# Performance work log

Hardware: AMD Instinct MI355X
Metric: run time of the kernel (lower is better)

The kernel has to match this reference:

```python
import jax, jax.numpy as jnp
import numpy as np

H_SIZE = 1024
N_HEADS = 16
D_K = H_SIZE // N_HEADS


def setup_inputs() -> dict:
    key = jax.random.key(0)
    ks = jax.random.split(key, 12)
    s = 1.0 / np.sqrt(H_SIZE)
    inp = {
        "x": jax.random.normal(ks[0], (2, 2048, H_SIZE), dtype=jnp.float32),
        "Wq": jax.random.uniform(ks[1], (H_SIZE, H_SIZE), minval=-s, maxval=s),
        "bq": jax.random.uniform(ks[2], (H_SIZE,), minval=-s, maxval=s),
        "Wk": jax.random.uniform(ks[3], (H_SIZE, H_SIZE), minval=-s, maxval=s),
        "bk": jax.random.uniform(ks[4], (H_SIZE,), minval=-s, maxval=s),
        "Wv": jax.random.uniform(ks[5], (H_SIZE, H_SIZE), minval=-s, maxval=s),
        "bv": jax.random.uniform(ks[6], (H_SIZE,), minval=-s, maxval=s),
        "Wo": jax.random.uniform(ks[7], (H_SIZE, H_SIZE), minval=-s, maxval=s),
        "bo": jax.random.uniform(ks[8], (H_SIZE,), minval=-s, maxval=s),
        "ln_gamma": jnp.ones((H_SIZE,), dtype=jnp.float32),
        "ln_beta": jnp.zeros((H_SIZE,), dtype=jnp.float32),
    }
    return inp


def reference(x, Wq, bq, Wk, bk, Wv, bv, Wo, bo, ln_gamma, ln_beta):
    B, L, H = x.shape
    residual = x
    # QKV projections -> [B, n_heads, L, d_k]
    def proj(W, b):
        return (x @ W.T + b).reshape(B, L, N_HEADS, D_K).transpose(0, 2, 1, 3)
    q = proj(Wq, bq)
    k = proj(Wk, bk)
    v = proj(Wv, bv)
    # scaled dot-product attention (dropout = identity in eval mode)
    scores = jnp.einsum("bhqd,bhkd->bhqk", q, k) / jnp.sqrt(jnp.float32(D_K))
    attn = jax.nn.softmax(scores, axis=-1)
    out = jnp.einsum("bhqk,bhkd->bhqd", attn, v)
    out = out.transpose(0, 2, 1, 3).reshape(B, L, H)
    out = out @ Wo.T + bo
    # residual + LayerNorm
    y = out + residual
    mu = jnp.mean(y, axis=-1, keepdims=True)
    var = jnp.var(y, axis=-1, keepdims=True)
    y = (y - mu) / jnp.sqrt(var + 1e-5) * ln_gamma + ln_beta
    return y
```

## Files before the change

### kernel.cpp

```cpp
#include <hip/hip_runtime.h>

#define H_SIZE 1024
#define N_HEADS 16
#define D_K 64
#define SEQ 2048
#define BATCH 2
#define M_TOT 4096

typedef __bf16 __attribute__((ext_vector_type(8))) bf16_8;
typedef float __attribute__((ext_vector_type(4))) f32x4;
typedef float __attribute__((ext_vector_type(16))) f32x16;
typedef int __attribute__((ext_vector_type(4))) int4v;

#define SWZ(r) ((((r) & 7) ^ (((r) >> 3) & 7)))

__device__ __forceinline__ ushort f2bf(float f) {
    unsigned int u = __float_as_uint(f);
    unsigned int r = (u + 0x7FFFu + ((u >> 16) & 1u)) >> 16;
    return (ushort)r;
}

__device__ __forceinline__ unsigned int cvtpk(float lo, float hi) {
    unsigned int r;
    asm("v_cvt_pk_bf16_f32 %0, %1, %2" : "=v"(r) : "v"(lo), "v"(hi));
    return r;
}

__device__ __forceinline__ float exp2_raw(float x) {
    float r;
    asm("v_exp_f32 %0, %1" : "=v"(r) : "v"(x));
    return r;
}

__device__ __forceinline__ void gld16(void* lds, const void* g) {
    __builtin_amdgcn_global_load_lds(
        (const __attribute__((address_space(1))) unsigned int*)g,
        (__attribute__((address_space(3))) unsigned int*)lds, 16, 0, 0);
}

__global__ __launch_bounds__(256) void cast_all_kernel(
    const float* __restrict__ x, const float* __restrict__ wq, const float* __restrict__ wk,
    const float* __restrict__ wv, const float* __restrict__ wo,
    ushort* __restrict__ xb, ushort* __restrict__ wqb, ushort* __restrict__ wkb,
    ushort* __restrict__ wvb, ushort* __restrict__ wob) {
    int i = blockIdx.x * 256 + threadIdx.x;
    const float* src;
    ushort* dst;
    int off;
    if (i < 1048576) {
        src = x; dst = xb; off = i;
    } else {
        int j = i - 1048576;
        int w = j >> 18;
        off = j & 262143;
        src = (w == 0) ? wq : (w == 1) ? wk : (w == 2) ? wv : wo;
        dst = (w == 0) ? wqb : (w == 1) ? wkb : (w == 2) ? wvb : wob;
    }
    float4 v = ((const float4*)src)[off];
    ushort4 o;
    o.x = f2bf(v.x); o.y = f2bf(v.y); o.z = f2bf(v.z); o.w = f2bf(v.w);
    ((ushort4*)dst)[off] = o;
}

__global__ __launch_bounds__(256) void gemm_qkv(
    const ushort* __restrict__ A, const ushort* __restrict__ wq,
    const ushort* __restrict__ wk, const ushort* __restrict__ wv,
    const float* __restrict__ bq, const float* __restrict__ bk, const float* __restrict__ bv,
    ushort* __restrict__ Qb, ushort* __restrict__ Kb, ushort* __restrict__ Vtb) {
    constexpr int BK = 32;
    __shared__ ushort As[3][128 * BK];
    __shared__ ushort Bs[3][128 * BK];
    const int tid = threadIdx.x;
    const int lane = tid & 63, wid = tid >> 6;
    const int wr = wid >> 1, wc = wid & 1;
    const int hi = lane >> 4, lo = lane & 15;
    const int bm0 = blockIdx.x * 128;
    const int t3 = blockIdx.y >> 3;
    const int bn0 = (blockIdx.y & 7) * 128;
    const ushort* Bw = (t3 == 0) ? wq : (t3 == 1) ? wk : wv;
    const float* bias = (t3 == 0) ? bq : (t3 == 1) ? bk : bv;

    f32x4 acc[4][4] = {};

    const int srow = tid >> 2;
    const int sseg = ((tid & 3) ^ ((tid >> 3) & 3)) * 8;
    const ushort* gaB = A + (size_t)(bm0 + srow) * H_SIZE + sseg;
    const ushort* gbB = Bw + (size_t)(bn0 + srow) * H_SIZE + sseg;
    const int ldsOff = tid * 16;

#define STAGE(ba, bb, kt)                                 \
    {                                                     \
        char* la = (char*)(ba) + ldsOff;                  \
        char* lb = (char*)(bb) + ldsOff;                  \
        gld16(la, gaB + (kt));                            \
        gld16(la + 4096, gaB + 64 * H_SIZE + (kt));       \
        gld16(lb, gbB + (kt));                            \
        gld16(lb + 4096, gbB + 64 * H_SIZE + (kt));       \
    }

    STAGE(&As[0][0], &Bs[0][0], 0);
    STAGE(&As[1][0], &Bs[1][0], BK);
    asm volatile("s_waitcnt vmcnt(4)" ::: "memory");
    __builtin_amdgcn_s_barrier();
    __builtin_amdgcn_sched_barrier(0);

    constexpr int NT = H_SIZE / BK;
    const int rxv = (lo >> 1) & 3;
    int cur = 0;
    for (int t = 0; t < NT; t++) {
        int c2 = cur + 2; if (c2 >= 3) c2 -= 3;
        if (t + 2 < NT) STAGE(&As[c2][0], &Bs[c2][0], (t + 2) * BK);
        {
            bf16_8 af[4], bfv[4];
            const ushort* pa = &As[cur][(wr * 64 + lo) * BK + ((hi ^ rxv) * 8)];
            const ushort* pb = &Bs[cur][(wc * 64 + lo) * BK + ((hi ^ rxv) * 8)];
#pragma unroll
            for (int i = 0; i < 4; i++) af[i] = *(const bf16_8*)(pa + i * 16 * BK);
#pragma unroll
            for (int i = 0; i < 4; i++) bfv[i] = *(const bf16_8*)(pb + i * 16 * BK);
#pragma unroll
            for (int mi = 0; mi < 4; mi++)
#pragma unroll
                for (int ni = 0; ni < 4; ni++)
                    acc[mi][ni] = __builtin_amdgcn_mfma_f32_16x16x32_bf16(
                        af[mi], bfv[ni], acc[mi][ni], 0, 0, 0);
        }
        if (t + 1 < NT) {
            if (t + 2 < NT) { asm volatile("s_waitcnt vmcnt(4)" ::: "memory"); }
            else            { asm volatile("s_waitcnt vmcnt(0)" ::: "memory"); }
            __builtin_amdgcn_s_barrier();
            __builtin_amdgcn_sched_barrier(0);
        }
        cur = cur + 1; if (cur >= 3) cur -= 3;
    }
#undef STAGE

#pragma unroll
    for (int mi = 0; mi < 4; mi++) {
#pragma unroll
        for (int ni = 0; ni < 4; ni++) {
            const int row0 = bm0 + wr * 64 + mi * 16 + hi * 4;
            const int col = bn0 + wc * 64 + ni * 16 + lo;
            const float bv = bias[col];
            const int h = col >> 6, dk = col & 63;
            if (t3 == 2) {
                const int b = row0 >> 11, l0 = row0 & 2047;
                const int lsw0 = (l0 & ~63) | (((((l0 >> 3) & 7) ^ SWZ(dk)) & 7) << 3) | (l0 & 7);
                uint2 o;
                o.x = cvtpk(acc[mi][ni][0] + bv, acc[mi][ni][1] + bv);
                o.y = cvtpk(acc[mi][ni][2] + bv, acc[mi][ni][3] + bv);
                *(uint2*)&Vtb[((size_t)(b * N_HEADS + h) * D_K + dk) * SEQ + lsw0] = o;
            } else {
#pragma unroll
                for (int rr = 0; rr < 4; rr++) {
                    const int m = row0 + rr;
                    const int b = m >> 11, l = m & 2047;
                    float val = acc[mi][ni][rr] + bv;
                    if (t3 == 0) {
                        Qb[((size_t)(b * N_HEADS + h) * SEQ + l) * D_K + dk] =
                            f2bf(val * 0.18033688f);
                    } else {
                        int dks = ((((dk >> 3) ^ SWZ(l & 63)) & 7) << 3) | (dk & 7);
                        Kb[((size_t)(b * N_HEADS + h) * SEQ + l) * D_K + dks] = f2bf(val);
                    }
                }
            }
        }
    }
}

__global__ __launch_bounds__(256) void gemm_o(const ushort* __restrict__ A,
                                              const ushort* __restrict__ Bw,
                                              const float* __restrict__ bias,
                                              const float* __restrict__ resid,
                                              float* __restrict__ outp) {
    constexpr int BK = 32;
    __shared__ ushort As[3][128 * BK];
    __shared__ ushort Bs[3][64 * BK];
    const int tid = threadIdx.x;
    const int lane = tid & 63, wid = tid >> 6;
    const int wr = wid >> 1, wc = wid & 1;
    const int hi = lane >> 4, lo = lane & 15;
    const int bm0 = blockIdx.x * 128, bn0 = blockIdx.y * 64;

    f32x4 acc[4][2] = {};

    const int srow = tid >> 2;
    const int sseg = ((tid & 3) ^ ((tid >> 3) & 3)) * 8;
    const ushort* gaB = A + (size_t)(bm0 + srow) * H_SIZE + sseg;
    const ushort* gbB = Bw + (size_t)(bn0 + srow) * H_SIZE + sseg;
    const int ldsOff = tid * 16;

#define STAGE(ba, bb, kt)                                 \
    {                                                     \
        char* la = (char*)(ba) + ldsOff;                  \
        gld16(la, gaB + (kt));                            \
        gld16(la + 4096, gaB + 64 * H_SIZE + (kt));       \
        gld16((char*)(bb) + ldsOff, gbB + (kt));          \
    }

    STAGE(&As[0][0], &Bs[0][0], 0);
    STAGE(&As[1][0], &Bs[1][0], BK);
    asm volatile("s_waitcnt vmcnt(3)" ::: "memory");
    __builtin_amdgcn_s_barrier();
    __builtin_amdgcn_sched_barrier(0);

    constexpr int NT = H_SIZE / BK;
    const int rxv = (lo >> 1) & 3;
    int cur = 0;
    for (int t = 0; t < NT; t++) {
        int c2 = cur + 2; if (c2 >= 3) c2 -= 3;
        if (t + 2 < NT) STAGE(&As[c2][0], &Bs[c2][0], (t + 2) * BK);
        {
            bf16_8 af[4], bfv[2];
            const ushort* pa = &As[cur][(wr * 64 + lo) * BK + ((hi ^ rxv) * 8)];
            const ushort* pb = &Bs[cur][(wc * 32 + lo) * BK + ((hi ^ rxv) * 8)];
#pragma unroll
            for (int i = 0; i < 4; i++) af[i] = *(const bf16_8*)(pa + i * 16 * BK);
#pragma unroll
            for (int i = 0; i < 2; i++) bfv[i] = *(const bf16_8*)(pb + i * 16 * BK);
#pragma unroll
            for (int mi = 0; mi < 4; mi++)
#pragma unroll
                for (int ni = 0; ni < 2; ni++)
                    acc[mi][ni] = __builtin_amdgcn_mfma_f32_16x16x32_bf16(
                        af[mi], bfv[ni], acc[mi][ni], 0, 0, 0);
        }
        if (t + 1 < NT) {
            if (t + 2 < NT) { asm volatile("s_waitcnt vmcnt(3)" ::: "memory"); }
            else            { asm volatile("s_waitcnt vmcnt(0)" ::: "memory"); }
            __builtin_amdgcn_s_barrier();
            __builtin_amdgcn_sched_barrier(0);
        }
        cur = cur + 1; if (cur >= 3) cur -= 3;
    }
#undef STAGE

#pragma unroll
    for (int mi = 0; mi < 4; mi++) {
#pragma unroll
        for (int ni = 0; ni < 2; ni++) {
            const int row0 = bm0 + wr * 64 + mi * 16 + hi * 4;
            const int col = bn0 + wc * 32 + ni * 16 + lo;
            const float bv = bias[col];
#pragma unroll
            for (int rr = 0; rr < 4; rr++) {
                const int m = row0 + rr;
                outp[(size_t)m * H_SIZE + col] =
                    acc[mi][ni][rr] + bv + resid[(size_t)m * H_SIZE + col];
            }
        }
    }
}

__global__ __launch_bounds__(256) void attn_kernel(const ushort* __restrict__ Q,
                                                   const ushort* __restrict__ Ksw,
                                                   const ushort* __restrict__ Vsw,
                                                   ushort* __restrict__ Op0,
                                                   ushort* __restrict__ Op1,
                                                   float* __restrict__ Lpart) {
    __shared__ ushort Ks[2][64 * 64];
    __shared__ ushort Vs[2][64 * 64];
    const int lane = threadIdx.x & 63, wid = threadIdx.x >> 6;
    const int h32 = lane >> 5, q32 = lane & 31;
    const int bh = blockIdx.y;
    const int z = blockIdx.z;
    const int q0w = blockIdx.x * 128 + wid * 32;
    const int kbase = z * (SEQ / 2);
    const ushort* Qh = Q + (size_t)bh * SEQ * D_K;
    const ushort* Kp = Ksw + (size_t)bh * SEQ * D_K;
    const ushort* Vp = Vsw + (size_t)bh * D_K * SEQ;

    bf16_8 qf[4];
#pragma unroll
    for (int tt = 0; tt < 4; tt++)
        qf[tt] = *(const bf16_8*)(Qh + (size_t)(q0w + q32) * D_K + tt * 16 + h32 * 8);

    bf16_8 onesf;
#pragma unroll
    for (int i = 0; i < 8; i++) onesf[i] = (__bf16)1.0f;

    f32x16 oacc0 = {}, oacc1 = {}, lsacc = {};

    const int koff = wid * 2048 + lane * 16;
    const int vrow = wid * 16 + (lane >> 3);
    const int vseg = (lane & 7) * 16;

#define STAGE(bb, kt)                                                             \
    {                                                                             \
        const char* kg = (const char*)(Kp + (size_t)(kt) * D_K);                  \
        char* kl = (char*)&Ks[bb][0];                                             \
        gld16(kl + koff, kg + koff);                                              \
        gld16(kl + koff + 1024, kg + koff + 1024);                                \
        char* vl = (char*)&Vs[bb][0];                                             \
        gld16(vl + vrow * 128 + vseg,                                             \
              (const char*)(Vp + (size_t)vrow * SEQ + (kt)) + vseg);              \
        gld16(vl + (vrow + 8) * 128 + vseg,                                       \
              (const char*)(Vp + (size_t)(vrow + 8) * SEQ + (kt)) + vseg);        \
    }

    STAGE(0, kbase);
    __syncthreads();
    int buf = 0;
    constexpr int NTT = (SEQ / 2) / 64;
    for (int t = 0; t < NTT; t++) {
        if (t + 1 < NTT) STAGE(buf ^ 1, kbase + (t + 1) * 64);
        const ushort* kb = &Ks[buf][0];
        const ushort* vb = &Vs[buf][0];
#pragma unroll
        for (int kh = 0; kh < 2; kh++) {
            f32x16 st = {};
            const int krow = kh * 32 + q32;
            __builtin_amdgcn_s_setprio(1);
#pragma unroll
            for (int tt = 0; tt < 4; tt++) {
                int sg = (2 * tt + h32) ^ SWZ(krow);
                bf16_8 kf = *(const bf16_8*)(kb + krow * 64 + sg * 8);
                st = __builtin_amdgcn_mfma_f32_32x32x16_bf16(kf, qf[tt], st, 0, 0, 0);
            }
            __builtin_amdgcn_s_setprio(0);
            float p[16];
#pragma unroll
            for (int rr = 0; rr < 16; rr++) p[rr] = exp2_raw(st[rr]);

            union { unsigned int w[4]; bf16_8 v; } pf0, pf1;
#pragma unroll
            for (int i = 0; i < 2; i++) {
                unsigned int a = cvtpk(p[2 * i], p[2 * i + 1]);
                unsigned int b = cvtpk(p[4 + 2 * i], p[4 + 2 * i + 1]);
                asm volatile("v_permlane32_swap_b32 %0, %1" : "+v"(a), "+v"(b));
                pf0.w[i] = a; pf0.w[2 + i] = b;
                unsigned int c = cvtpk(p[8 + 2 * i], p[8 + 2 * i + 1]);
                unsigned int d = cvtpk(p[12 + 2 * i], p[12 + 2 * i + 1]);
                asm volatile("v_permlane32_swap_b32 %0, %1" : "+v"(c), "+v"(d));
                pf1.w[i] = c; pf1.w[2 + i] = d;
            }

            __builtin_amdgcn_s_setprio(1);
            lsacc = __builtin_amdgcn_mfma_f32_32x32x16_bf16(pf0.v, onesf, lsacc, 0, 0, 0);
            lsacc = __builtin_amdgcn_mfma_f32_32x32x16_bf16(pf1.v, onesf, lsacc, 0, 0, 0);
            {
                const int vr0 = q32;
                int sg0 = (4 * kh + h32) ^ SWZ(vr0);
                int sg1 = (4 * kh + 2 + h32) ^ SWZ(vr0);
                bf16_8 vf0 = *(const bf16_8*)(vb + vr0 * 64 + sg0 * 8);
                bf16_8 vf1 = *(const bf16_8*)(vb + vr0 * 64 + sg1 * 8);
                oacc0 = __builtin_amdgcn_mfma_f32_32x32x16_bf16(pf0.v, vf0, oacc0, 0, 0, 0);
                oacc0 = __builtin_amdgcn_mfma_f32_32x32x16_bf16(pf1.v, vf1, oacc0, 0, 0, 0);
            }
            {
                const int vr1 = 32 + q32;
                int sg0 = (4 * kh + h32) ^ SWZ(vr1);
                int sg1 = (4 * kh + 2 + h32) ^ SWZ(vr1);
                bf16_8 vf0 = *(const bf16_8*)(vb + vr1 * 64 + sg0 * 8);
                bf16_8 vf1 = *(const bf16_8*)(vb + vr1 * 64 + sg1 * 8);
                oacc1 = __builtin_amdgcn_mfma_f32_32x32x16_bf16(pf0.v, vf0, oacc1, 0, 0, 0);
                oacc1 = __builtin_amdgcn_mfma_f32_32x32x16_bf16(pf1.v, vf1, oacc1, 0, 0, 0);
            }
            __builtin_amdgcn_s_setprio(0);
        }
        __syncthreads();
        buf ^= 1;
    }
#undef STAGE

    ushort* Op = (z == 0) ? Op0 : Op1;
    float* Lp = Lpart + (size_t)z * N_HEADS * BATCH * SEQ;
    const int b = bh >> 4, h = bh & 15;
#pragma unroll
    for (int rr = 0; rr < 16; rr++) {
        const int qloc = (rr & 3) + 8 * (rr >> 2) + 4 * h32;
        const int l = q0w + qloc;
        ushort* orow = Op + ((size_t)(b * SEQ + l)) * H_SIZE + h * 64;
        orow[q32] = f2bf(oacc0[rr]);
        orow[32 + q32] = f2bf(oacc1[rr]);
        if (q32 == 0) Lp[(size_t)bh * SEQ + l] = lsacc[rr];
    }
}

__global__ __launch_bounds__(256) void combine_kernel(const ushort* __restrict__ O0,
                                                      const ushort* __restrict__ O1,
                                                      const float* __restrict__ Lp,
                                                      ushort* __restrict__ Ao) {
    int idx = blockIdx.x * 256 + threadIdx.x;
    int m = idx >> 7;
    int col0 = (idx & 127) * 8;
    int b = m >> 11, l = m & 2047, h = col0 >> 6;
    int bh = b * N_HEADS + h;
    float inv = 1.0f / (Lp[(size_t)bh * SEQ + l] +
                        Lp[(size_t)(N_HEADS * BATCH + bh) * SEQ + l]);
    size_t off = (size_t)m * H_SIZE + col0;
    int4v a = *(const int4v*)(O0 + off);
    int4v c = *(const int4v*)(O1 + off);
    unsigned int r[4];
#pragma unroll
    for (int j = 0; j < 4; j++) {
        unsigned int ua = (unsigned int)a[j], uc = (unsigned int)c[j];
        float lo = __uint_as_float(ua << 16) + __uint_as_float(uc << 16);
        float hi = __uint_as_float(ua & 0xFFFF0000u) + __uint_as_float(uc & 0xFFFF0000u);
        r[j] = cvtpk(lo * inv, hi * inv);
    }
    *(int4v*)(Ao + off) = *(const int4v*)r;
}

__global__ __launch_bounds__(256) void ln_kernel(float* __restrict__ y,
                                                 const float* __restrict__ gamma,
                                                 const float* __restrict__ beta) {
    const int row = blockIdx.x;
    float4* p = (float4*)(y + (size_t)row * H_SIZE);
    float4 v = p[threadIdx.x];
    float s = v.x + v.y + v.z + v.w;
    float s2 = v.x * v.x + v.y * v.y + v.z * v.z + v.w * v.w;
#pragma unroll
    for (int off = 1; off < 64; off <<= 1) {
        s += __shfl_xor(s, off);
        s2 += __shfl_xor(s2, off);
    }
    __shared__ float ss[4], ss2[4];
    const int wid = threadIdx.x >> 6, lane = threadIdx.x & 63;
    if (lane == 0) { ss[wid] = s; ss2[wid] = s2; }
    __syncthreads();
    s = ss[0] + ss[1] + ss[2] + ss[3];
    s2 = ss2[0] + ss2[1] + ss2[2] + ss2[3];
    const float mean = s * (1.0f / H_SIZE);
    const float var = s2 * (1.0f / H_SIZE) - mean * mean;
    const float rstd = rsqrtf(var + 1e-5f);
    const float4 g = ((const float4*)gamma)[threadIdx.x];
    const float4 bt = ((const float4*)beta)[threadIdx.x];
    float4 o;
    o.x = (v.x - mean) * rstd * g.x + bt.x;
    o.y = (v.y - mean) * rstd * g.y + bt.y;
    o.z = (v.z - mean) * rstd * g.z + bt.z;
    o.w = (v.w - mean) * rstd * g.w + bt.w;
    p[threadIdx.x] = o;
}

extern "C" void kernel_launch(void* const* d_in, const int* in_sizes, int n_in,
                              void* d_out, int out_size, void* d_ws, size_t ws_size,
                              hipStream_t stream) {
    const float* x = (const float*)d_in[0];
    const float* Wq = (const float*)d_in[1];
    const float* bq = (const float*)d_in[2];
    const float* Wk = (const float*)d_in[3];
    const float* bk = (const float*)d_in[4];
    const float* Wv = (const float*)d_in[5];
    const float* bv = (const float*)d_in[6];
    const float* Wo = (const float*)d_in[7];
    const float* bo = (const float*)d_in[8];
    const float* gamma = (const float*)d_in[9];
    const float* beta = (const float*)d_in[10];

    char* ws = (char*)d_ws;
    ushort* xb  = (ushort*)(ws);
    ushort* wqb = (ushort*)(ws + (8u << 20));
    ushort* wkb = (ushort*)(ws + (10u << 20));
    ushort* wvb = (ushort*)(ws + (12u << 20));
    ushort* wob = (ushort*)(ws + (14u << 20));
    ushort* Qb  = (ushort*)(ws + (16u << 20));
    ushort* Kb  = (ushort*)(ws + (24u << 20));
    ushort* Vtb = (ushort*)(ws + (32u << 20));
    ushort* Ao  = (ushort*)(ws + (40u << 20));
    ushort* Op0 = (ushort*)(ws);
    ushort* Op1 = Ao;
    float*  Lpt = (float*)(ws + (48u << 20));

    cast_all_kernel<<<8192, 256, 0, stream>>>(x, Wq, Wk, Wv, Wo, xb, wqb, wkb, wvb, wob);

    dim3 gq(M_TOT / 128, 24);
    gemm_qkv<<<gq, 256, 0, stream>>>(xb, wqb, wkb, wvb, bq, bk, bv, Qb, Kb, Vtb);

    dim3 g2(SEQ / 128, BATCH * N_HEADS, 2);
    attn_kernel<<<g2, 256, 0, stream>>>(Qb, Kb, Vtb, Op0, Op1, Lpt);

    combine_kernel<<<(M_TOT * H_SIZE / 8) / 256, 256, 0, stream>>>(Op0, Op1, Lpt, Ao);

    dim3 go(M_TOT / 128, H_SIZE / 64);
    gemm_o<<<go, 256, 0, stream>>>(Ao, wob, bo, x, (float*)d_out);

    ln_kernel<<<M_TOT, 256, 0, stream>>>((float*)d_out, gamma, beta);
}
```

Measured before the change: 142.4 us.

## Process two query tiles per wave with triple-buffered K/V and VALU row sums

Each wave now handles 64 query rows instead of 32, reusing every K and V fragment loaded from LDS across two query tiles and halving the grid. The K/V staging moves from double to triple buffering with explicit vmcnt waits and raw barriers, so loads run two tiles ahead. The softmax denominator is now summed on the VALU with a cross-half shuffle instead of extra MFMAs against a ones vector. In exchange the kernel needs more registers and LDS per block, and with only 512 blocks occupancy and load balance across CUs may drop.

```diff
diff --git a/kernel.cpp b/kernel.cpp
--- a/kernel.cpp
+++ b/kernel.cpp
@@ -259,28 +259,27 @@
                                                    ushort* __restrict__ Op0,
                                                    ushort* __restrict__ Op1,
                                                    float* __restrict__ Lpart) {
-    __shared__ ushort Ks[2][64 * 64];
-    __shared__ ushort Vs[2][64 * 64];
+    __shared__ ushort Ks[3][64 * 64];
+    __shared__ ushort Vs[3][64 * 64];
     const int lane = threadIdx.x & 63, wid = threadIdx.x >> 6;
     const int h32 = lane >> 5, q32 = lane & 31;
     const int bh = blockIdx.y;
     const int z = blockIdx.z;
-    const int q0w = blockIdx.x * 128 + wid * 32;
+    const int q0w = blockIdx.x * 256 + wid * 64;
     const int kbase = z * (SEQ / 2);
     const ushort* Qh = Q + (size_t)bh * SEQ * D_K;
     const ushort* Kp = Ksw + (size_t)bh * SEQ * D_K;
     const ushort* Vp = Vsw + (size_t)bh * D_K * SEQ;
 
-    bf16_8 qf[4];
-#pragma unroll
-    for (int tt = 0; tt < 4; tt++)
-        qf[tt] = *(const bf16_8*)(Qh + (size_t)(q0w + q32) * D_K + tt * 16 + h32 * 8);
-
-    bf16_8 onesf;
-#pragma unroll
-    for (int i = 0; i < 8; i++) onesf[i] = (__bf16)1.0f;
-
-    f32x16 oacc0 = {}, oacc1 = {}, lsacc = {};
+    bf16_8 qfA[4], qfB[4];
+#pragma unroll
+    for (int tt = 0; tt < 4; tt++) {
+        qfA[tt] = *(const bf16_8*)(Qh + (size_t)(q0w + q32) * D_K + tt * 16 + h32 * 8);
+        qfB[tt] = *(const bf16_8*)(Qh + (size_t)(q0w + 32 + q32) * D_K + tt * 16 + h32 * 8);
+    }
+
+    f32x16 oA0 = {}, oA1 = {}, oB0 = {}, oB1 = {};
+    float lsA = 0.f, lsB = 0.f;
 
     const int koff = wid * 2048 + lane * 16;
     const int vrow = wid * 16 + (lane >> 3);
@@ -300,53 +299,75 @@
     }
 
     STAGE(0, kbase);
-    __syncthreads();
-    int buf = 0;
+    STAGE(1, kbase + 64);
+    asm volatile("s_waitcnt vmcnt(4)" ::: "memory");
+    __builtin_amdgcn_s_barrier();
+    __builtin_amdgcn_sched_barrier(0);
+
     constexpr int NTT = (SEQ / 2) / 64;
+    int cur = 0;
     for (int t = 0; t < NTT; t++) {
-        if (t + 1 < NTT) STAGE(buf ^ 1, kbase + (t + 1) * 64);
-        const ushort* kb = &Ks[buf][0];
-        const ushort* vb = &Vs[buf][0];
+        int c2 = cur + 2; if (c2 >= 3) c2 -= 3;
+        if (t + 2 < NTT) STAGE(c2, kbase + (t + 2) * 64);
+        const ushort* kb = &Ks[cur][0];
+        const ushort* vb = &Vs[cur][0];
 #pragma unroll
         for (int kh = 0; kh < 2; kh++) {
-            f32x16 st = {};
+            f32x16 stA = {}, stB = {};
             const int krow = kh * 32 + q32;
             __builtin_amdgcn_s_setprio(1);
 #pragma unroll
             for (int tt = 0; tt < 4; tt++) {
                 int sg = (2 * tt + h32) ^ SWZ(krow);
                 bf16_8 kf = *(const bf16_8*)(kb + krow * 64 + sg * 8);
-                st = __builtin_amdgcn_mfma_f32_32x32x16_bf16(kf, qf[tt], st, 0, 0, 0);
+                stA = __builtin_amdgcn_mfma_f32_32x32x16_bf16(kf, qfA[tt], stA, 0, 0, 0);
+                stB = __builtin_amdgcn_mfma_f32_32x32x16_bf16(kf, qfB[tt], stB, 0, 0, 0);
             }
             __builtin_amdgcn_s_setprio(0);
-            float p[16];
-#pragma unroll
-            for (int rr = 0; rr < 16; rr++) p[rr] = exp2_raw(st[rr]);
-
-            union { unsigned int w[4]; bf16_8 v; } pf0, pf1;
+
+            union { unsigned int w[4]; bf16_8 v; } pfA0, pfA1, pfB0, pfB1;
+            float partA = 0.f, partB = 0.f;
 #pragma unroll
             for (int i = 0; i < 2; i++) {
-                unsigned int a = cvtpk(p[2 * i], p[2 * i + 1]);
-                unsigned int b = cvtpk(p[4 + 2 * i], p[4 + 2 * i + 1]);
-                asm volatile("v_permlane32_swap_b32 %0, %1" : "+v"(a), "+v"(b));
-                pf0.w[i] = a; pf0.w[2 + i] = b;
-                unsigned int c = cvtpk(p[8 + 2 * i], p[8 + 2 * i + 1]);
-                unsigned int d = cvtpk(p[12 + 2 * i], p[12 + 2 * i + 1]);
-                asm volatile("v_permlane32_swap_b32 %0, %1" : "+v"(c), "+v"(d));
-                pf1.w[i] = c; pf1.w[2 + i] = d;
+                float a0 = exp2_raw(stA[2 * i]),     a1 = exp2_raw(stA[2 * i + 1]);
+                float a2 = exp2_raw(stA[4 + 2 * i]), a3 = exp2_raw(stA[4 + 2 * i + 1]);
+                partA += (a0 + a1) + (a2 + a3);
+                unsigned int ua = cvtpk(a0, a1), ub = cvtpk(a2, a3);
+                asm volatile("v_permlane32_swap_b32 %0, %1" : "+v"(ua), "+v"(ub));
+                pfA0.w[i] = ua; pfA0.w[2 + i] = ub;
+                float a4 = exp2_raw(stA[8 + 2 * i]),  a5 = exp2_raw(stA[8 + 2 * i + 1]);
+                float a6 = exp2_raw(stA[12 + 2 * i]), a7 = exp2_raw(stA[12 + 2 * i + 1]);
+                partA += (a4 + a5) + (a6 + a7);
+                unsigned int uc = cvtpk(a4, a5), ud = cvtpk(a6, a7);
+                asm volatile("v_permlane32_swap_b32 %0, %1" : "+v"(uc), "+v"(ud));
+                pfA1.w[i] = uc; pfA1.w[2 + i] = ud;
+                float b0 = exp2_raw(stB[2 * i]),     b1 = exp2_raw(stB[2 * i + 1]);
+                float b2 = exp2_raw(stB[4 + 2 * i]), b3 = exp2_raw(stB[4 + 2 * i + 1]);
+                partB += (b0 + b1) + (b2 + b3);
+                unsigned int ue = cvtpk(b0, b1), uf = cvtpk(b2, b3);
+                asm volatile("v_permlane32_swap_b32 %0, %1" : "+v"(ue), "+v"(uf));
+                pfB0.w[i] = ue; pfB0.w[2 + i] = uf;
+                float b4 = exp2_raw(stB[8 + 2 * i]),  b5 = exp2_raw(stB[8 + 2 * i + 1]);
+                float b6 = exp2_raw(stB[12 + 2 * i]), b7 = exp2_raw(stB[12 + 2 * i + 1]);
+                partB += (b4 + b5) + (b6 + b7);
+                unsigned int ug = cvtpk(b4, b5), uh = cvtpk(b6, b7);
+                asm volatile("v_permlane32_swap_b32 %0, %1" : "+v"(ug), "+v"(uh));
+                pfB1.w[i] = ug; pfB1.w[2 + i] = uh;
             }
+            lsA += partA + __shfl_xor(partA, 32);
+            lsB += partB + __shfl_xor(partB, 32);
 
             __builtin_amdgcn_s_setprio(1);
-            lsacc = __builtin_amdgcn_mfma_f32_32x32x16_bf16(pf0.v, onesf, lsacc, 0, 0, 0);
-            lsacc = __builtin_amdgcn_mfma_f32_32x32x16_bf16(pf1.v, onesf, lsacc, 0, 0, 0);
             {
                 const int vr0 = q32;
                 int sg0 = (4 * kh + h32) ^ SWZ(vr0);
                 int sg1 = (4 * kh + 2 + h32) ^ SWZ(vr0);
                 bf16_8 vf0 = *(const bf16_8*)(vb + vr0 * 64 + sg0 * 8);
                 bf16_8 vf1 = *(const bf16_8*)(vb + vr0 * 64 + sg1 * 8);
-                oacc0 = __builtin_amdgcn_mfma_f32_32x32x16_bf16(pf0.v, vf0, oacc0, 0, 0, 0);
-                oacc0 = __builtin_amdgcn_mfma_f32_32x32x16_bf16(pf1.v, vf1, oacc0, 0, 0, 0);
+                oA0 = __builtin_amdgcn_mfma_f32_32x32x16_bf16(pfA0.v, vf0, oA0, 0, 0, 0);
+                oB0 = __builtin_amdgcn_mfma_f32_32x32x16_bf16(pfB0.v, vf0, oB0, 0, 0, 0);
+                oA0 = __builtin_amdgcn_mfma_f32_32x32x16_bf16(pfA1.v, vf1, oA0, 0, 0, 0);
+                oB0 = __builtin_amdgcn_mfma_f32_32x32x16_bf16(pfB1.v, vf1, oB0, 0, 0, 0);
             }
             {
                 const int vr1 = 32 + q32;
@@ -354,13 +375,20 @@
                 int sg1 = (4 * kh + 2 + h32) ^ SWZ(vr1);
                 bf16_8 vf0 = *(const bf16_8*)(vb + vr1 * 64 + sg0 * 8);
                 bf16_8 vf1 = *(const bf16_8*)(vb + vr1 * 64 + sg1 * 8);
-                oacc1 = __builtin_amdgcn_mfma_f32_32x32x16_bf16(pf0.v, vf0, oacc1, 0, 0, 0);
-                oacc1 = __builtin_amdgcn_mfma_f32_32x32x16_bf16(pf1.v, vf1, oacc1, 0, 0, 0);
+                oA1 = __builtin_amdgcn_mfma_f32_32x32x16_bf16(pfA0.v, vf0, oA1, 0, 0, 0);
+                oB1 = __builtin_amdgcn_mfma_f32_32x32x16_bf16(pfB0.v, vf0, oB1, 0, 0, 0);
+                oA1 = __builtin_amdgcn_mfma_f32_32x32x16_bf16(pfA1.v, vf1, oA1, 0, 0, 0);
+                oB1 = __builtin_amdgcn_mfma_f32_32x32x16_bf16(pfB1.v, vf1, oB1, 0, 0, 0);
             }
             __builtin_amdgcn_s_setprio(0);
         }
-        __syncthreads();
-        buf ^= 1;
+        if (t + 1 < NTT) {
+            if (t + 2 < NTT) { asm volatile("s_waitcnt vmcnt(4)" ::: "memory"); }
+            else             { asm volatile("s_waitcnt vmcnt(0)" ::: "memory"); }
+            __builtin_amdgcn_s_barrier();
+            __builtin_amdgcn_sched_barrier(0);
+        }
+        cur = cur + 1; if (cur >= 3) cur -= 3;
     }
 #undef STAGE
 
@@ -370,11 +398,18 @@
 #pragma unroll
     for (int rr = 0; rr < 16; rr++) {
         const int qloc = (rr & 3) + 8 * (rr >> 2) + 4 * h32;
-        const int l = q0w + qloc;
-        ushort* orow = Op + ((size_t)(b * SEQ + l)) * H_SIZE + h * 64;
-        orow[q32] = f2bf(oacc0[rr]);
-        orow[32 + q32] = f2bf(oacc1[rr]);
-        if (q32 == 0) Lp[(size_t)bh * SEQ + l] = lsacc[rr];
+        const int lA = q0w + qloc;
+        ushort* orowA = Op + ((size_t)(b * SEQ + lA)) * H_SIZE + h * 64;
+        orowA[q32] = f2bf(oA0[rr]);
+        orowA[32 + q32] = f2bf(oA1[rr]);
+        const int lB = q0w + 32 + qloc;
+        ushort* orowB = Op + ((size_t)(b * SEQ + lB)) * H_SIZE + h * 64;
+        orowB[q32] = f2bf(oB0[rr]);
+        orowB[32 + q32] = f2bf(oB1[rr]);
+    }
+    if (lane < 32) {
+        Lp[(size_t)bh * SEQ + q0w + q32] = lsA;
+        Lp[(size_t)bh * SEQ + q0w + 32 + q32] = lsB;
     }
 }
 
@@ -469,7 +504,7 @@
     dim3 gq(M_TOT / 128, 24);
     gemm_qkv<<<gq, 256, 0, stream>>>(xb, wqb, wkb, wvb, bq, bk, bv, Qb, Kb, Vtb);
 
-    dim3 g2(SEQ / 128, BATCH * N_HEADS, 2);
+    dim3 g2(SEQ / 256, BATCH * N_HEADS, 2);
     attn_kernel<<<g2, 256, 0, stream>>>(Qb, Kb, Vtb, Op0, Op1, Lpt);
 
     combine_kernel<<<(M_TOT * H_SIZE / 8) / 256, 256, 0, stream>>>(Op0, Op1, Lpt, Ao);
```

Result: faster. 137.9 us (-3.1%).
